# Kernel tuning notes

Hardware: AMD Instinct MI355X
Metric: run time of the kernel (lower is better)

Reference implementation:

```python
import jax, jax.numpy as jnp
import numpy as np

N = 50000
E = 800000
IN_DIM = 256
HID = 128
OUT = 64


def setup_inputs() -> dict:
    key = jax.random.key(0)
    ks = jax.random.split(key, 12)
    inp = {}
    inp["x"] = jax.random.normal(ks[0], (N, IN_DIM), dtype=jnp.float32)
    inp["edge_index"] = jax.random.randint(ks[1], (2, E), 0, N, dtype=jnp.int64)
    s0 = 1.0 / np.sqrt(IN_DIM)
    inp["W0"] = jax.random.uniform(ks[2], (IN_DIM, HID), jnp.float32, -s0, s0)
    inp["b0"] = jax.random.uniform(ks[3], (HID,), jnp.float32, -s0, s0)
    sa = 1.0 / np.sqrt(2 * HID)
    inp["att_w1"] = jax.random.uniform(ks[4], (2 * HID, 1), jnp.float32, -sa, sa)
    inp["att_b1"] = jax.random.uniform(ks[5], (1,), jnp.float32, -sa, sa)
    inp["eps1"] = jnp.float32(0.1)
    inp["att_w2"] = jax.random.uniform(ks[6], (2 * HID, 1), jnp.float32, -sa, sa)
    inp["att_b2"] = jax.random.uniform(ks[7], (1,), jnp.float32, -sa, sa)
    inp["eps2"] = jnp.float32(0.1)
    sc = 1.0 / np.sqrt(HID)
    inp["Wc"] = jax.random.uniform(ks[8], (HID, OUT), jnp.float32, -sc, sc)
    inp["bc"] = jax.random.uniform(ks[9], (OUT,), jnp.float32, -sc, sc)
    return inp


def _fagcn_layer(x, row, col, att_w, att_b, eps):
    # x: [N, H]; row/col: [E]
    x_i = x[row]                       # [E, H] source (gathered)
    x_j = x[col]                       # [E, H] destination
    # cat([x_i, x_j]) @ att_w == x_i @ att_w[:H] + x_j @ att_w[H:]
    H = x.shape[1]
    score = x_i @ att_w[:H] + x_j @ att_w[H:] + att_b  # [E, 1]
    alpha = jnp.tanh(score)            # [E, 1]
    messages = alpha * x_i             # [E, H]
    agg = jax.ops.segment_sum(messages, col, num_segments=x.shape[0])  # [N, H]
    return eps * x + (1.0 - eps) * agg


def reference(x, edge_index, W0, b0, att_w1, att_b1, eps1, att_w2, att_b2, eps2, Wc, bc):
    row, col = edge_index[0], edge_index[1]
    h = jax.nn.relu(x @ W0 + b0)       # initial linear + relu (dropout=eval identity)
    h = jax.nn.relu(_fagcn_layer(h, row, col, att_w1, att_b1, eps1))
    h = jax.nn.relu(_fagcn_layer(h, row, col, att_w2, att_b2, eps2))
    return h @ Wc + bc                 # [N, OUT]
```

## Files before the change

### kernel.cpp

```cpp
#include <hip/hip_runtime.h>

#define N_NODES 50000
#define E_EDGES 800000
#define IN_DIM 256
#define HID 128
#define OUT_DIM 64
#define SLOT 64

typedef unsigned short u16;
typedef __attribute__((ext_vector_type(8))) short short8;
typedef __attribute__((ext_vector_type(4))) float floatx4;

__device__ __forceinline__ u16 f2bf(float f) {
    unsigned u = __float_as_uint(f);
    unsigned r = (u + 0x7FFFu + ((u >> 16) & 1u)) >> 16;
    return (u16)r;
}
__device__ __forceinline__ void bf8_unpack(uint4 v, float* f) {
    f[0] = __uint_as_float(v.x << 16); f[1] = __uint_as_float(v.x & 0xffff0000u);
    f[2] = __uint_as_float(v.y << 16); f[3] = __uint_as_float(v.y & 0xffff0000u);
    f[4] = __uint_as_float(v.z << 16); f[5] = __uint_as_float(v.z & 0xffff0000u);
    f[6] = __uint_as_float(v.w << 16); f[7] = __uint_as_float(v.w & 0xffff0000u);
}
__device__ __forceinline__ uint4 bf8_pack(const float* f) {
    uint4 o;
    o.x = f2bf(f[0]) | ((unsigned)f2bf(f[1]) << 16);
    o.y = f2bf(f[2]) | ((unsigned)f2bf(f[3]) << 16);
    o.z = f2bf(f[4]) | ((unsigned)f2bf(f[5]) << 16);
    o.w = f2bf(f[6]) | ((unsigned)f2bf(f[7]) << 16);
    return o;
}

__global__ __launch_bounds__(256) void k_build(const int* __restrict__ ei,
                                               int* __restrict__ cnt,
                                               u16* __restrict__ srcidx,
                                               const float* __restrict__ Wc,
                                               u16* __restrict__ Wct) {
    const int gid = blockIdx.x * 256 + threadIdx.x;
    if (gid < HID * OUT_DIM)
        Wct[gid] = f2bf(Wc[(gid & 127) * OUT_DIM + (gid >> 7)]);
    if (gid >= E_EDGES / 8) return;
    const int4 w0 = ((const int4*)ei)[2 * gid];
    const int4 w1 = ((const int4*)ei)[2 * gid + 1];
    const int4 c0 = ((const int4*)(ei + E_EDGES))[2 * gid];
    const int4 c1 = ((const int4*)(ei + E_EDGES))[2 * gid + 1];
    const int p0 = atomicAdd(&cnt[c0.x], 1);
    const int p1 = atomicAdd(&cnt[c0.y], 1);
    const int p2 = atomicAdd(&cnt[c0.z], 1);
    const int p3 = atomicAdd(&cnt[c0.w], 1);
    const int p4 = atomicAdd(&cnt[c1.x], 1);
    const int p5 = atomicAdd(&cnt[c1.y], 1);
    const int p6 = atomicAdd(&cnt[c1.z], 1);
    const int p7 = atomicAdd(&cnt[c1.w], 1);
    if (p0 < SLOT) srcidx[(c0.x << 6) + p0] = (u16)w0.x;
    if (p1 < SLOT) srcidx[(c0.y << 6) + p1] = (u16)w0.y;
    if (p2 < SLOT) srcidx[(c0.z << 6) + p2] = (u16)w0.z;
    if (p3 < SLOT) srcidx[(c0.w << 6) + p3] = (u16)w0.w;
    if (p4 < SLOT) srcidx[(c1.x << 6) + p4] = (u16)w1.x;
    if (p5 < SLOT) srcidx[(c1.y << 6) + p5] = (u16)w1.y;
    if (p6 < SLOT) srcidx[(c1.z << 6) + p6] = (u16)w1.z;
    if (p7 < SLOT) srcidx[(c1.w << 6) + p7] = (u16)w1.w;
}

#define LR 64
#define KS 64
#define KP 72

__global__ __launch_bounds__(256) void k_lin(
    const float* __restrict__ x, const float* __restrict__ W0,
    const float* __restrict__ b0, const float* __restrict__ aw1,
    u16* __restrict__ h, float* __restrict__ sa, float* __restrict__ sb) {
    __shared__ u16 As[LR][KP];
    __shared__ u16 Bs[HID][KP];
    const int t = threadIdx.x;
    const int lane = t & 63;
    const int w = t >> 6;
    const int sub = lane & 15;
    const int quad = lane >> 4;
    const int row0 = blockIdx.x * LR;

    floatx4 acc[8];
    #pragma unroll
    for (int i = 0; i < 8; ++i) acc[i] = (floatx4){0.f, 0.f, 0.f, 0.f};

    const int ar = t >> 2;
    const int ak = (t & 3) * 16;
    const int sr = t >> 1;
    const int sk = (t & 1) * 32;

    for (int k0 = 0; k0 < IN_DIM; k0 += KS) {
        {
            int gr = row0 + ar;
            if (gr > N_NODES - 1) gr = N_NODES - 1;
            const float* src = x + (size_t)gr * IN_DIM + k0 + ak;
            #pragma unroll
            for (int i = 0; i < 2; ++i) {
                float4 f0 = ((const float4*)src)[2 * i];
                float4 f1 = ((const float4*)src)[2 * i + 1];
                uint4 p;
                p.x = f2bf(f0.x) | ((unsigned)f2bf(f0.y) << 16);
                p.y = f2bf(f0.z) | ((unsigned)f2bf(f0.w) << 16);
                p.z = f2bf(f1.x) | ((unsigned)f2bf(f1.y) << 16);
                p.w = f2bf(f1.z) | ((unsigned)f2bf(f1.w) << 16);
                *(uint4*)&As[ar][ak + 8 * i] = p;
            }
            const float* wp = W0 + (size_t)(k0 + sk) * HID + sr;
            #pragma unroll
            for (int i = 0; i < 4; ++i) {
                uint4 p;
                unsigned q[4];
                #pragma unroll
                for (int j = 0; j < 4; ++j) {
                    const float lo = wp[(i * 8 + 2 * j) * HID];
                    const float hi = wp[(i * 8 + 2 * j + 1) * HID];
                    q[j] = f2bf(lo) | ((unsigned)f2bf(hi) << 16);
                }
                p.x = q[0]; p.y = q[1]; p.z = q[2]; p.w = q[3];
                *(uint4*)&Bs[sr][sk + 8 * i] = p;
            }
        }
        __syncthreads();
        #pragma unroll
        for (int kk = 0; kk < KS; kk += 32) {
            short8 a0 = *(const short8*)&As[w * 16 + sub][kk + quad * 8];
            #pragma unroll
            for (int ct = 0; ct < 8; ++ct) {
                short8 bb = *(const short8*)&Bs[ct * 16 + sub][kk + quad * 8];
                acc[ct] = __builtin_amdgcn_mfma_f32_16x16x32_bf16(a0, bb, acc[ct], 0, 0, 0);
            }
        }
        __syncthreads();
    }

    float bias[8], w1c[8], w2c[8];
    #pragma unroll
    for (int ct = 0; ct < 8; ++ct) {
        const int col = ct * 16 + sub;
        bias[ct] = b0[col];
        w1c[ct] = aw1[col];
        w2c[ct] = aw1[HID + col];
    }
    #pragma unroll
    for (int reg = 0; reg < 4; ++reg) {
        const int gr = row0 + w * 16 + quad * 4 + reg;
        const bool ok = gr < N_NODES;
        float ps = 0.f, pd = 0.f;
        #pragma unroll
        for (int ct = 0; ct < 8; ++ct) {
            const float val = fmaxf(acc[ct][reg] + bias[ct], 0.f);
            if (ok) h[(size_t)gr * HID + ct * 16 + sub] = f2bf(val);
            ps += val * w1c[ct];
            pd += val * w2c[ct];
        }
        #pragma unroll
        for (int off = 1; off < 16; off <<= 1) {
            ps += __shfl_xor(ps, off);
            pd += __shfl_xor(pd, off);
        }
        if (sub == 0 && ok) { sa[gr] = ps; sb[gr] = pd; }
    }
}

__global__ __launch_bounds__(256) void k_agg(const u16* __restrict__ hin,
                                             const float* __restrict__ sa,
                                             const float* __restrict__ sb,
                                             const float* __restrict__ attb,
                                             const float* __restrict__ epsp,
                                             const int* __restrict__ cnt,
                                             const u16* __restrict__ srcidx,
                                             u16* __restrict__ hout,
                                             const float* __restrict__ attw_next,
                                             float* __restrict__ sa_next,
                                             float* __restrict__ sb_next) {
    const int qid = threadIdx.x >> 4;
    const int sub = threadIdx.x & 15;
    const int n = blockIdx.x * 16 + qid;
    if (n >= N_NODES) return;
    const float b = attb[0];
    const float sbn = sb[n];
    const int beg = n << 6;
    int deg = cnt[n];
    if (deg > SLOT) deg = SLOT;
    const int end = beg + deg;
    float acc[8];
    #pragma unroll
    for (int j = 0; j < 8; ++j) acc[j] = 0.f;

    int e = beg;
    for (; e + 8 <= end; e += 8) {
        int s[8];
        #pragma unroll
        for (int i = 0; i < 8; ++i) s[i] = srcidx[e + i];
        uint4 v[8];
        #pragma unroll
        for (int i = 0; i < 8; ++i)
            v[i] = *(const uint4*)(hin + (size_t)s[i] * HID + sub * 8);
        float al[8];
        #pragma unroll
        for (int i = 0; i < 8; ++i) al[i] = tanhf(sa[s[i]] + sbn + b);
        #pragma unroll
        for (int i = 0; i < 8; ++i) {
            float f[8];
            bf8_unpack(v[i], f);
            #pragma unroll
            for (int j = 0; j < 8; ++j) acc[j] += al[i] * f[j];
        }
    }
    for (; e < end; ++e) {
        const int s = srcidx[e];
        const float a = tanhf(sa[s] + sbn + b);
        const uint4 v = *(const uint4*)(hin + (size_t)s * HID + sub * 8);
        float f[8];
        bf8_unpack(v, f);
        #pragma unroll
        for (int j = 0; j < 8; ++j) acc[j] += a * f[j];
    }

    const float eps = epsp[0];
    const float om = 1.f - eps;
    const uint4 sv = *(const uint4*)(hin + (size_t)n * HID + sub * 8);
    float self[8], hv[8];
    bf8_unpack(sv, self);
    #pragma unroll
    for (int j = 0; j < 8; ++j)
        hv[j] = fmaxf(eps * self[j] + om * acc[j], 0.f);
    *(uint4*)(hout + (size_t)n * HID + sub * 8) = bf8_pack(hv);

    if (attw_next != nullptr) {
        float psum = 0.f, dsum = 0.f;
        #pragma unroll
        for (int j = 0; j < 8; ++j) {
            psum += hv[j] * attw_next[sub * 8 + j];
            dsum += hv[j] * attw_next[HID + sub * 8 + j];
        }
        #pragma unroll
        for (int off = 1; off < 16; off <<= 1) {
            psum += __shfl_xor(psum, off);
            dsum += __shfl_xor(dsum, off);
        }
        if (sub == 0) { sa_next[n] = psum; sb_next[n] = dsum; }
    }
}

#define HP 136

__global__ __launch_bounds__(256) void k_out_mfma(const u16* __restrict__ h,
                                                  const u16* __restrict__ Wct,
                                                  const float* __restrict__ bc,
                                                  float* __restrict__ out) {
    __shared__ u16 Hs[LR][HP];
    const int t = threadIdx.x;
    const int lane = t & 63;
    const int w = t >> 6;
    const int sub = lane & 15;
    const int quad = lane >> 4;
    const int row0 = blockIdx.x * LR;

    {
        const int hr = t >> 2;
        const int hc = (t & 3) * 32;
        int gr = row0 + hr;
        if (gr > N_NODES - 1) gr = N_NODES - 1;
        const u16* src = h + (size_t)gr * HID + hc;
        #pragma unroll
        for (int i = 0; i < 4; ++i)
            *(uint4*)&Hs[hr][hc + 8 * i] = ((const uint4*)src)[i];
    }
    __syncthreads();

    floatx4 acc[4];
    #pragma unroll
    for (int j = 0; j < 4; ++j) acc[j] = (floatx4){0.f, 0.f, 0.f, 0.f};

    #pragma unroll
    for (int ks = 0; ks < 4; ++ks) {
        const int ko = ks * 32 + quad * 8;
        short8 a = *(const short8*)&Hs[w * 16 + sub][ko];
        #pragma unroll
        for (int ct = 0; ct < 4; ++ct) {
            short8 bb = *(const short8*)(Wct + (ct * 16 + sub) * HID + ko);
            acc[ct] = __builtin_amdgcn_mfma_f32_16x16x32_bf16(a, bb, acc[ct], 0, 0, 0);
        }
    }

    #pragma unroll
    for (int ct = 0; ct < 4; ++ct) {
        const float bias = bc[ct * 16 + sub];
        #pragma unroll
        for (int reg = 0; reg < 4; ++reg) {
            const int gr = row0 + w * 16 + quad * 4 + reg;
            if (gr < N_NODES)
                out[(size_t)gr * OUT_DIM + ct * 16 + sub] = acc[ct][reg] + bias;
        }
    }
}

extern "C" void kernel_launch(void* const* d_in, const int* in_sizes, int n_in,
                              void* d_out, int out_size, void* d_ws, size_t ws_size,
                              hipStream_t stream) {
    const float* x   = (const float*)d_in[0];
    const int*   ei  = (const int*)d_in[1];
    const float* W0  = (const float*)d_in[2];
    const float* b0  = (const float*)d_in[3];
    const float* aw1 = (const float*)d_in[4];
    const float* ab1 = (const float*)d_in[5];
    const float* e1  = (const float*)d_in[6];
    const float* aw2 = (const float*)d_in[7];
    const float* ab2 = (const float*)d_in[8];
    const float* e2  = (const float*)d_in[9];
    const float* Wc  = (const float*)d_in[10];
    const float* bc  = (const float*)d_in[11];
    float* out = (float*)d_out;

    u16* hA  = (u16*)d_ws;
    u16* hB  = hA + (size_t)N_NODES * HID;
    u16* Wct = hB + (size_t)N_NODES * HID;
    float* sa1 = (float*)(Wct + HID * OUT_DIM);
    float* sb1 = sa1 + N_NODES;
    float* sa2 = sb1 + N_NODES;
    float* sb2 = sa2 + N_NODES;
    int* cnt    = (int*)(sb2 + N_NODES);
    u16* srcidx = (u16*)(cnt + N_NODES);

    hipMemsetAsync(cnt, 0, N_NODES * sizeof(int), stream);
    k_build<<<(E_EDGES / 8 + 255) / 256, 256, 0, stream>>>(ei, cnt, srcidx, Wc, Wct);
    k_lin<<<(N_NODES + LR - 1) / LR, 256, 0, stream>>>(x, W0, b0, aw1, hA, sa1, sb1);
    k_agg<<<(N_NODES + 15) / 16, 256, 0, stream>>>(hA, sa1, sb1, ab1, e1, cnt, srcidx,
                                                   hB, aw2, sa2, sb2);
    k_agg<<<(N_NODES + 15) / 16, 256, 0, stream>>>(hB, sa2, sb2, ab2, e2, cnt, srcidx,
                                                   hA, nullptr, nullptr, nullptr);
    k_out_mfma<<<(N_NODES + LR - 1) / LR, 256, 0, stream>>>(hA, Wct, bc, out);
}
```

Measured before the change: 283.4 us.

## Merge edge bucketing into linear kernel and vectorize aggregation index/tanh loads

Merges the edge-bucketing kernel and the first linear MFMA kernel into one launch, with block ranges split by role so both run concurrently. In the aggregation kernel, the eight source indices are loaded as one 16-byte vector and prefetched one iteration ahead. Each lane now computes one tanh, and the values are shared with __shfl instead of every lane computing all eight. The scalar tail loop becomes a masked batch of up to eight edges. The fused kernel reserves the linear kernel's shared memory even for build blocks, which may reduce occupancy.

```diff
diff --git a/kernel.cpp b/kernel.cpp
--- a/kernel.cpp
+++ b/kernel.cpp
@@ -6,6 +6,14 @@
 #define HID 128
 #define OUT_DIM 64
 #define SLOT 64
+
+#define LR 64
+#define KS 64
+#define KP 72
+#define HP 136
+
+#define NBUILD ((E_EDGES / 8 + 255) / 256)
+#define NLIN ((N_NODES + LR - 1) / LR)
 
 typedef unsigned short u16;
 typedef __attribute__((ext_vector_type(8))) short short8;
@@ -31,53 +39,50 @@
     return o;
 }
 
-__global__ __launch_bounds__(256) void k_build(const int* __restrict__ ei,
-                                               int* __restrict__ cnt,
-                                               u16* __restrict__ srcidx,
-                                               const float* __restrict__ Wc,
-                                               u16* __restrict__ Wct) {
-    const int gid = blockIdx.x * 256 + threadIdx.x;
-    if (gid < HID * OUT_DIM)
-        Wct[gid] = f2bf(Wc[(gid & 127) * OUT_DIM + (gid >> 7)]);
-    if (gid >= E_EDGES / 8) return;
-    const int4 w0 = ((const int4*)ei)[2 * gid];
-    const int4 w1 = ((const int4*)ei)[2 * gid + 1];
-    const int4 c0 = ((const int4*)(ei + E_EDGES))[2 * gid];
-    const int4 c1 = ((const int4*)(ei + E_EDGES))[2 * gid + 1];
-    const int p0 = atomicAdd(&cnt[c0.x], 1);
-    const int p1 = atomicAdd(&cnt[c0.y], 1);
-    const int p2 = atomicAdd(&cnt[c0.z], 1);
-    const int p3 = atomicAdd(&cnt[c0.w], 1);
-    const int p4 = atomicAdd(&cnt[c1.x], 1);
-    const int p5 = atomicAdd(&cnt[c1.y], 1);
-    const int p6 = atomicAdd(&cnt[c1.z], 1);
-    const int p7 = atomicAdd(&cnt[c1.w], 1);
-    if (p0 < SLOT) srcidx[(c0.x << 6) + p0] = (u16)w0.x;
-    if (p1 < SLOT) srcidx[(c0.y << 6) + p1] = (u16)w0.y;
-    if (p2 < SLOT) srcidx[(c0.z << 6) + p2] = (u16)w0.z;
-    if (p3 < SLOT) srcidx[(c0.w << 6) + p3] = (u16)w0.w;
-    if (p4 < SLOT) srcidx[(c1.x << 6) + p4] = (u16)w1.x;
-    if (p5 < SLOT) srcidx[(c1.y << 6) + p5] = (u16)w1.y;
-    if (p6 < SLOT) srcidx[(c1.z << 6) + p6] = (u16)w1.z;
-    if (p7 < SLOT) srcidx[(c1.w << 6) + p7] = (u16)w1.w;
-}
-
-#define LR 64
-#define KS 64
-#define KP 72
-
-__global__ __launch_bounds__(256) void k_lin(
+__global__ __launch_bounds__(256) void k_front(
     const float* __restrict__ x, const float* __restrict__ W0,
     const float* __restrict__ b0, const float* __restrict__ aw1,
-    u16* __restrict__ h, float* __restrict__ sa, float* __restrict__ sb) {
+    u16* __restrict__ h, float* __restrict__ sa, float* __restrict__ sb,
+    const int* __restrict__ ei, int* __restrict__ cnt,
+    u16* __restrict__ srcidx, const float* __restrict__ Wc,
+    u16* __restrict__ Wct) {
     __shared__ u16 As[LR][KP];
     __shared__ u16 Bs[HID][KP];
+
+    if (blockIdx.x < NBUILD) {
+        const int gid = blockIdx.x * 256 + threadIdx.x;
+        if (gid < HID * OUT_DIM)
+            Wct[gid] = f2bf(Wc[(gid & 127) * OUT_DIM + (gid >> 7)]);
+        if (gid >= E_EDGES / 8) return;
+        const int4 w0 = ((const int4*)ei)[2 * gid];
+        const int4 w1 = ((const int4*)ei)[2 * gid + 1];
+        const int4 c0 = ((const int4*)(ei + E_EDGES))[2 * gid];
+        const int4 c1 = ((const int4*)(ei + E_EDGES))[2 * gid + 1];
+        const int p0 = atomicAdd(&cnt[c0.x], 1);
+        const int p1 = atomicAdd(&cnt[c0.y], 1);
+        const int p2 = atomicAdd(&cnt[c0.z], 1);
+        const int p3 = atomicAdd(&cnt[c0.w], 1);
+        const int p4 = atomicAdd(&cnt[c1.x], 1);
+        const int p5 = atomicAdd(&cnt[c1.y], 1);
+        const int p6 = atomicAdd(&cnt[c1.z], 1);
+        const int p7 = atomicAdd(&cnt[c1.w], 1);
+        if (p0 < SLOT) srcidx[(c0.x << 6) + p0] = (u16)w0.x;
+        if (p1 < SLOT) srcidx[(c0.y << 6) + p1] = (u16)w0.y;
+        if (p2 < SLOT) srcidx[(c0.z << 6) + p2] = (u16)w0.z;
+        if (p3 < SLOT) srcidx[(c0.w << 6) + p3] = (u16)w0.w;
+        if (p4 < SLOT) srcidx[(c1.x << 6) + p4] = (u16)w1.x;
+        if (p5 < SLOT) srcidx[(c1.y << 6) + p5] = (u16)w1.y;
+        if (p6 < SLOT) srcidx[(c1.z << 6) + p6] = (u16)w1.z;
+        if (p7 < SLOT) srcidx[(c1.w << 6) + p7] = (u16)w1.w;
+        return;
+    }
+
     const int t = threadIdx.x;
     const int lane = t & 63;
     const int w = t >> 6;
     const int sub = lane & 15;
     const int quad = lane >> 4;
-    const int row0 = blockIdx.x * LR;
+    const int row0 = (blockIdx.x - NBUILD) * LR;
 
     floatx4 acc[8];
     #pragma unroll
@@ -187,17 +192,24 @@
     for (int j = 0; j < 8; ++j) acc[j] = 0.f;
 
     int e = beg;
+    uint4 svn;
+    if (e + 8 <= end) svn = *(const uint4*)(srcidx + e);
     for (; e + 8 <= end; e += 8) {
+        const uint4 sv = svn;
+        if (e + 16 <= end) svn = *(const uint4*)(srcidx + e + 8);
         int s[8];
-        #pragma unroll
-        for (int i = 0; i < 8; ++i) s[i] = srcidx[e + i];
+        s[0] = (int)(sv.x & 0xffffu); s[1] = (int)(sv.x >> 16);
+        s[2] = (int)(sv.y & 0xffffu); s[3] = (int)(sv.y >> 16);
+        s[4] = (int)(sv.z & 0xffffu); s[5] = (int)(sv.z >> 16);
+        s[6] = (int)(sv.w & 0xffffu); s[7] = (int)(sv.w >> 16);
         uint4 v[8];
         #pragma unroll
         for (int i = 0; i < 8; ++i)
             v[i] = *(const uint4*)(hin + (size_t)s[i] * HID + sub * 8);
+        const float tt = tanhf(sa[s[sub & 7]] + sbn + b);
         float al[8];
         #pragma unroll
-        for (int i = 0; i < 8; ++i) al[i] = tanhf(sa[s[i]] + sbn + b);
+        for (int i = 0; i < 8; ++i) al[i] = __shfl(tt, i, 16);
         #pragma unroll
         for (int i = 0; i < 8; ++i) {
             float f[8];
@@ -206,14 +218,26 @@
             for (int j = 0; j < 8; ++j) acc[j] += al[i] * f[j];
         }
     }
-    for (; e < end; ++e) {
-        const int s = srcidx[e];
-        const float a = tanhf(sa[s] + sbn + b);
-        const uint4 v = *(const uint4*)(hin + (size_t)s * HID + sub * 8);
-        float f[8];
-        bf8_unpack(v, f);
-        #pragma unroll
-        for (int j = 0; j < 8; ++j) acc[j] += a * f[j];
+    const int rem = end - e;
+    if (rem > 0) {
+        const int sfirst = (int)srcidx[e];
+        int s[8];
+        #pragma unroll
+        for (int i = 0; i < 8; ++i) s[i] = (i < rem) ? (int)srcidx[e + i] : sfirst;
+        const float tt = ((sub & 7) < rem) ? tanhf(sa[s[sub & 7]] + sbn + b) : 0.f;
+        float al[8];
+        #pragma unroll
+        for (int i = 0; i < 8; ++i) al[i] = __shfl(tt, i, 16);
+        #pragma unroll
+        for (int i = 0; i < 8; ++i) {
+            if (i < rem) {
+                const uint4 v = *(const uint4*)(hin + (size_t)s[i] * HID + sub * 8);
+                float f[8];
+                bf8_unpack(v, f);
+                #pragma unroll
+                for (int j = 0; j < 8; ++j) acc[j] += al[i] * f[j];
+            }
+        }
     }
 
     const float eps = epsp[0];
@@ -241,8 +265,6 @@
         if (sub == 0) { sa_next[n] = psum; sb_next[n] = dsum; }
     }
 }
-
-#define HP 136
 
 __global__ __launch_bounds__(256) void k_out_mfma(const u16* __restrict__ h,
                                                   const u16* __restrict__ Wct,
@@ -323,8 +345,8 @@
     u16* srcidx = (u16*)(cnt + N_NODES);
 
     hipMemsetAsync(cnt, 0, N_NODES * sizeof(int), stream);
-    k_build<<<(E_EDGES / 8 + 255) / 256, 256, 0, stream>>>(ei, cnt, srcidx, Wc, Wct);
-    k_lin<<<(N_NODES + LR - 1) / LR, 256, 0, stream>>>(x, W0, b0, aw1, hA, sa1, sb1);
+    k_front<<<NBUILD + NLIN, 256, 0, stream>>>(x, W0, b0, aw1, hA, sa1, sb1,
+                                               ei, cnt, srcidx, Wc, Wct);
     k_agg<<<(N_NODES + 15) / 16, 256, 0, stream>>>(hA, sa1, sb1, ab1, e1, cnt, srcidx,
                                                    hB, aw2, sa2, sb2);
     k_agg<<<(N_NODES + 15) / 16, 256, 0, stream>>>(hB, sa2, sb2, ab2, e2, cnt, srcidx,
```

Measured after the change: 243.5 us. 14.1% less time.
